# Performance work log

Hardware: AMD Instinct MI355X
Metric: run time of the kernel (lower is better)

## Reference

```python
import jax, jax.numpy as jnp
import numpy as np

B, N, C = 8, 4096, 768
H = 12
D = C // H  # 64


def setup_inputs() -> dict:
    key = jax.random.key(0)
    k1, k2, k3 = jax.random.split(key, 3)
    x = jax.random.normal(k1, (B, N, C), dtype=jnp.float32)
    Wqkv = jax.random.normal(k2, (C, 3 * C), dtype=jnp.float32) * (C ** -0.5)
    Wproj = jax.random.normal(k3, (C, C), dtype=jnp.float32) * (C ** -0.5)
    bproj = jnp.zeros((C,), dtype=jnp.float32)
    return {"x": x, "Wqkv": Wqkv, "Wproj": Wproj, "bproj": bproj}


def reference(x, Wqkv, Wproj, bproj):
    b, n, c = x.shape
    qkv = x @ Wqkv  # [B,N,3C]
    qkv = qkv.reshape(b, n, 3, H, D).transpose(2, 0, 3, 1, 4)  # [3,B,H,N,D]
    q, k, v = qkv[0], qkv[1], qkv[2]
    # softmax over the sequence axis (dim=-2 in torch => N)
    k = jax.nn.softmax(k, axis=-2)
    # context: [B,H,D,D] -- small d x d intermediate
    context = jnp.einsum('bhnd,bhne->bhde', k, v)
    out = jnp.einsum('bhnd,bhde->bhne', q, context)  # [B,H,N,D]
    out = out.transpose(0, 2, 1, 3).reshape(b, n, c)  # b h n d -> b n (h d)
    return out @ Wproj + bproj
```

## Files before the change

kernel.cpp:

```cpp
#include <hip/hip_runtime.h>
#include <cstdint>
#include <cstddef>


typedef __bf16 bf8_t __attribute__((ext_vector_type(8)));
typedef float f4_t __attribute__((ext_vector_type(4)));
typedef float f16_t __attribute__((ext_vector_type(16)));

#define DEV_INLINE __device__ __forceinline__

DEV_INLINE void gload16(const void* g, void* l) {
  __builtin_amdgcn_global_load_lds(
      (const __attribute__((address_space(1))) void*)g,
      (__attribute__((address_space(3))) void*)l, 16, 0, 0);
}

__global__ __launch_bounds__(256) void cast_f32_bf16(const float* __restrict__ in,
                                                     __bf16* __restrict__ out, int n4) {
  int i = blockIdx.x * 256 + threadIdx.x;
  if (i >= n4) return;
  float4 f = ((const float4*)in)[i];
  union { __bf16 h[4]; uint2 u; } o;
  o.h[0] = (__bf16)f.x; o.h[1] = (__bf16)f.y; o.h[2] = (__bf16)f.z; o.h[3] = (__bf16)f.w;
  ((uint2*)out)[i] = o.u;
}

__global__ __launch_bounds__(256) void transpose_cast(const float* __restrict__ in,
                                                      __bf16* __restrict__ out, int R, int C) {
  __shared__ float t[64][65];
  const int tilesR = R >> 6;
  const int tr = blockIdx.x % tilesR, tc = blockIdx.x / tilesR;
  const int tx = threadIdx.x & 63, ty = threadIdx.x >> 6;
  const int r0 = tr * 64, c0 = tc * 64;
#pragma unroll
  for (int p = 0; p < 16; p++) {
    int r = p * 4 + ty;
    t[r][tx] = in[(size_t)(r0 + r) * C + c0 + tx];
  }
  __syncthreads();
#pragma unroll
  for (int p = 0; p < 16; p++) {
    int c = p * 4 + ty;
    out[(size_t)(c0 + c) * R + r0 + tx] = (__bf16)t[tx][c];
  }
}

__global__ __launch_bounds__(256) void wq_cast(const float* __restrict__ in,
                                               __bf16* __restrict__ out) {
  int o = blockIdx.x * 256 + threadIdx.x;
  int r = o / 768, c = o - r * 768;
  out[o] = (__bf16)in[r * 2304 + c];
}

__global__ __launch_bounds__(256) void gemm1_kv(const __bf16* __restrict__ A,
                                                const __bf16* __restrict__ B,
                                                __bf16* __restrict__ KTo,
                                                __bf16* __restrict__ VTo) {
  constexpr int LDA = 768, LDB = 768, KTOT = 768;
  __shared__ __bf16 sA[128 * 32];
  __shared__ __bf16 sB[128 * 32];
  const int tid = threadIdx.x;
  const int xcd = blockIdx.x & 7, g = blockIdx.x >> 3;
  const int mt = xcd * 32 + g / 12, nt = g % 12;
  const int lane = tid & 63, wv = tid >> 6;
  const int wr = (wv >> 1) * 64, wc = (wv & 1) * 64;
  const int l31 = lane & 31, l5 = lane >> 5;

  const int srow = tid >> 2;
  const int sk = ((tid & 3) ^ ((srow >> 1) & 3)) * 8;
  const __bf16* gA = A + (size_t)(mt * 128 + srow) * LDA + sk;
  const __bf16* gB = B + (size_t)(nt * 128 + srow) * LDB + sk;

  const int arow = wr + l31, brow = wc + l31;
  const int asw = (arow >> 1) & 3, bsw = (brow >> 1) & 3;
  const int aoff  = arow * 32 + ((l5 ^ asw) * 8);
  const int aoff2 = arow * 32 + (((2 | l5) ^ asw) * 8);
  const int boff  = brow * 32 + ((l5 ^ bsw) * 8);
  const int boff2 = brow * 32 + (((2 | l5) ^ bsw) * 8);

  f16_t acc[2][2];
#pragma unroll
  for (int i = 0; i < 2; i++)
#pragma unroll
    for (int j = 0; j < 2; j++)
#pragma unroll
      for (int e = 0; e < 16; e++) acc[i][j][e] = 0.f;

  for (int k0 = 0; k0 < KTOT; k0 += 32) {
    gload16(gA, &sA[tid * 8]);
    gload16(gA + 64 * LDA, &sA[tid * 8 + 2048]);
    gload16(gB, &sB[tid * 8]);
    gload16(gB + 64 * LDB, &sB[tid * 8 + 2048]);
    gA += 32; gB += 32;
    __syncthreads();
    bf8_t a0 = *(const bf8_t*)&sA[aoff];
    bf8_t a1 = *(const bf8_t*)&sA[aoff + 1024];
    bf8_t b0 = *(const bf8_t*)&sB[boff];
    bf8_t b1 = *(const bf8_t*)&sB[boff + 1024];
    acc[0][0] = __builtin_amdgcn_mfma_f32_32x32x16_bf16(a0, b0, acc[0][0], 0, 0, 0);
    acc[0][1] = __builtin_amdgcn_mfma_f32_32x32x16_bf16(a0, b1, acc[0][1], 0, 0, 0);
    acc[1][0] = __builtin_amdgcn_mfma_f32_32x32x16_bf16(a1, b0, acc[1][0], 0, 0, 0);
    acc[1][1] = __builtin_amdgcn_mfma_f32_32x32x16_bf16(a1, b1, acc[1][1], 0, 0, 0);
    a0 = *(const bf8_t*)&sA[aoff2];
    a1 = *(const bf8_t*)&sA[aoff2 + 1024];
    b0 = *(const bf8_t*)&sB[boff2];
    b1 = *(const bf8_t*)&sB[boff2 + 1024];
    acc[0][0] = __builtin_amdgcn_mfma_f32_32x32x16_bf16(a0, b0, acc[0][0], 0, 0, 0);
    acc[0][1] = __builtin_amdgcn_mfma_f32_32x32x16_bf16(a0, b1, acc[0][1], 0, 0, 0);
    acc[1][0] = __builtin_amdgcn_mfma_f32_32x32x16_bf16(a1, b0, acc[1][0], 0, 0, 0);
    acc[1][1] = __builtin_amdgcn_mfma_f32_32x32x16_bf16(a1, b1, acc[1][1], 0, 0, 0);
    __syncthreads();
  }

  const int s = nt / 6;
  __bf16* T = (s == 0) ? KTo : VTo;
  const int row0 = mt * 128 + wr;
  const int bidx = row0 >> 12;
  const int n0 = (row0 & 4095) + 4 * l5;
  const int colw0 = (nt % 6) * 128 + wc;
#pragma unroll
  for (int j = 0; j < 2; j++) {
    int cw = colw0 + j * 32 + l31;
    int h = cw >> 6, d = cw & 63;
    __bf16* Tp = &T[((size_t)(bidx * 12 + h) * 64 + d) * 4096];
#pragma unroll
    for (int i = 0; i < 2; i++) {
      int nb = n0 + i * 32;
#pragma unroll
      for (int r2 = 0; r2 < 4; r2++) {
        union { __bf16 h4[4]; uint2 u; } pk;
#pragma unroll
        for (int r = 0; r < 4; r++) pk.h4[r] = (__bf16)acc[i][j][r2 * 4 + r];
        *(uint2*)&Tp[nb + 8 * r2] = pk.u;
      }
    }
  }
}

__global__ __launch_bounds__(256) void stats_rows(const __bf16* __restrict__ KT,
                                                  float2* __restrict__ stats) {
  __shared__ float red[8];
  const __bf16* p = KT + (size_t)blockIdx.x * 4096;
  const int tid = threadIdx.x, lane = tid & 63, wv = tid >> 6;
  bf8_t x0 = *(const bf8_t*)&p[tid * 16];
  bf8_t x1 = *(const bf8_t*)&p[tid * 16 + 8];
  float v[16];
#pragma unroll
  for (int k = 0; k < 8; k++) { v[k] = (float)x0[k]; v[8 + k] = (float)x1[k]; }
  float m = v[0];
#pragma unroll
  for (int k = 1; k < 16; k++) m = fmaxf(m, v[k]);
  for (int o = 32; o; o >>= 1) m = fmaxf(m, __shfl_xor(m, o, 64));
  if (lane == 0) red[wv] = m;
  __syncthreads();
  m = fmaxf(fmaxf(red[0], red[1]), fmaxf(red[2], red[3]));
  float s = 0.f;
#pragma unroll
  for (int k = 0; k < 16; k++) s += __expf(v[k] - m);
  for (int o = 32; o; o >>= 1) s += __shfl_xor(s, o, 64);
  if (lane == 0) red[4 + wv] = s;
  __syncthreads();
  if (tid == 0) {
    float st = red[4] + red[5] + red[6] + red[7];
    stats[blockIdx.x] = make_float2(m, 1.0f / st);
  }
}

__global__ __launch_bounds__(256) void ctx_kernel(const __bf16* __restrict__ KT,
                                                  const __bf16* __restrict__ VT,
                                                  const float2* __restrict__ stats,
                                                  float* __restrict__ part) {
  const int bh = blockIdx.x >> 3, kc = blockIdx.x & 7;
  const int tid = threadIdx.x, lane = tid & 63, wv = tid >> 6;
  const int wr = (wv >> 1) * 32, wc = (wv & 1) * 32;
  const int lr = lane & 15, quad = lane >> 4;
  const __bf16* Ab = KT + (size_t)bh * 64 * 4096;
  const __bf16* Bb = VT + (size_t)bh * 64 * 4096;
  float2 st[2];
  st[0] = stats[bh * 64 + wr + lr];
  st[1] = stats[bh * 64 + wr + 16 + lr];
  const f4_t fz = {0.f, 0.f, 0.f, 0.f};
  f4_t acc[2][2] = {{fz, fz}, {fz, fz}};
  const int kbeg = kc * 512;
  for (int k0 = kbeg; k0 < kbeg + 512; k0 += 32) {
    bf8_t a[2], b[2];
#pragma unroll
    for (int i = 0; i < 2; i++) {
      bf8_t raw = *(const bf8_t*)&Ab[(size_t)(wr + i * 16 + lr) * 4096 + k0 + quad * 8];
#pragma unroll
      for (int e = 0; e < 8; e++)
        a[i][e] = (__bf16)(__expf((float)raw[e] - st[i].x) * st[i].y);
    }
#pragma unroll
    for (int j = 0; j < 2; j++)
      b[j] = *(const bf8_t*)&Bb[(size_t)(wc + j * 16 + lr) * 4096 + k0 + quad * 8];
#pragma unroll
    for (int i = 0; i < 2; i++)
#pragma unroll
      for (int j = 0; j < 2; j++)
        acc[i][j] = __builtin_amdgcn_mfma_f32_16x16x32_bf16(a[i], b[j], acc[i][j], 0, 0, 0);
  }
  float* po = part + (size_t)blockIdx.x * 4096;
#pragma unroll
  for (int i = 0; i < 2; i++)
#pragma unroll
    for (int j = 0; j < 2; j++)
#pragma unroll
      for (int r = 0; r < 4; r++)
        po[(wr + i * 16 + quad * 4 + r) * 64 + wc + j * 16 + lr] = acc[i][j][r];
}

__global__ __launch_bounds__(256) void wfused_kernel(const float* __restrict__ part,
                                                     const __bf16* __restrict__ WpT,
                                                     __bf16* __restrict__ B2T) {
  __shared__ __bf16 sctx[64 * 64];
  const int bh = blockIdx.x, cblk = blockIdx.y;
  const int b = bh / 12, h = bh % 12;
  const int tid = threadIdx.x;
  for (int i = tid; i < 4096; i += 256) {
    float s = 0.f;
#pragma unroll
    for (int kc = 0; kc < 8; kc++) s += part[(size_t)(bh * 8 + kc) * 4096 + i];
    sctx[i] = (__bf16)s;
  }
  __syncthreads();
  const int lane = tid & 63, wv = tid >> 6, lr = lane & 15, quad = lane >> 4;
  const int c0 = cblk * 192 + wv * 48;
  const f4_t fz = {0.f, 0.f, 0.f, 0.f};
  f4_t acc[3][4];
#pragma unroll
  for (int i = 0; i < 3; i++)
#pragma unroll
    for (int j = 0; j < 4; j++) acc[i][j] = fz;
#pragma unroll
  for (int k0 = 0; k0 < 64; k0 += 32) {
    bf8_t a[3], bq[4];
#pragma unroll
    for (int i = 0; i < 3; i++)
      a[i] = *(const bf8_t*)&WpT[(size_t)(c0 + i * 16 + lr) * 768 + h * 64 + k0 + quad * 8];
#pragma unroll
    for (int j = 0; j < 4; j++)
      bq[j] = *(const bf8_t*)&sctx[(j * 16 + lr) * 64 + k0 + quad * 8];
#pragma unroll
    for (int i = 0; i < 3; i++)
#pragma unroll
      for (int j = 0; j < 4; j++)
        acc[i][j] = __builtin_amdgcn_mfma_f32_16x16x32_bf16(a[i], bq[j], acc[i][j], 0, 0, 0);
  }
#pragma unroll
  for (int i = 0; i < 3; i++)
#pragma unroll
    for (int j = 0; j < 4; j++)
#pragma unroll
      for (int r = 0; r < 4; r++) {
        int c = c0 + i * 16 + quad * 4 + r;
        int d = j * 16 + lr;
        B2T[((size_t)b * 768 + c) * 768 + h * 64 + d] = (__bf16)acc[i][j][r];
      }
}

__global__ __launch_bounds__(256) void combine_kernel(const __bf16* __restrict__ B2Tall,
                                                      const __bf16* __restrict__ Wq,
                                                      __bf16* __restrict__ Wcomb) {
  constexpr int LD = 768, BK = 32, KTOT = 768;
  __shared__ __bf16 sA[64 * 32];
  __shared__ __bf16 sB[64 * 32];
  const int b = blockIdx.x / 144, rem = blockIdx.x % 144;
  const int mt = rem / 12, nt = rem % 12;
  const __bf16* A = B2Tall + (size_t)b * 768 * 768;
  const int tid = threadIdx.x, lane = tid & 63, wv = tid >> 6;
  const int wr = (wv >> 1) * 32, wc = (wv & 1) * 32;
  const int lr = lane & 15, quad = lane >> 4;

  const int e0 = tid * 8;
  const int srow = e0 >> 5, skk = e0 & 31;
  const __bf16* gA = A + (size_t)(mt * 64 + srow) * LD + skk;
  const __bf16* gB = Wq + (size_t)(nt * 64 + srow) * LD + skk;

  const f4_t fz = {0.f, 0.f, 0.f, 0.f};
  f4_t acc[2][2] = {{fz, fz}, {fz, fz}};

  for (int k0 = 0; k0 < KTOT; k0 += BK) {
    gload16(gA, &sA[e0]);
    gload16(gB, &sB[e0]);
    gA += BK; gB += BK;
    __syncthreads();
    bf8_t a[2], bq[2];
#pragma unroll
    for (int i = 0; i < 2; i++)
      a[i] = *(const bf8_t*)&sA[(wr + i * 16 + lr) * 32 + quad * 8];
#pragma unroll
    for (int j = 0; j < 2; j++)
      bq[j] = *(const bf8_t*)&sB[(wc + j * 16 + lr) * 32 + quad * 8];
#pragma unroll
    for (int i = 0; i < 2; i++)
#pragma unroll
      for (int j = 0; j < 2; j++)
        acc[i][j] = __builtin_amdgcn_mfma_f32_16x16x32_bf16(a[i], bq[j], acc[i][j], 0, 0, 0);
    __syncthreads();
  }
  __bf16* C = Wcomb + (size_t)b * 768 * 768;
  const int row0 = mt * 64 + wr, col0 = nt * 64 + wc;
#pragma unroll
  for (int i = 0; i < 2; i++)
#pragma unroll
    for (int j = 0; j < 2; j++)
#pragma unroll
      for (int r = 0; r < 4; r++)
        C[(size_t)(row0 + i * 16 + quad * 4 + r) * 768 + col0 + j * 16 + lr] =
            (__bf16)acc[i][j][r];
}

__global__ __launch_bounds__(256) void gemm2_out(const __bf16* __restrict__ A,
                                                 const __bf16* __restrict__ Ball,
                                                 float* __restrict__ C,
                                                 const float* __restrict__ bias) {
  constexpr int LDA = 768, LDB = 768, KTOT = 768;
  __shared__ __bf16 sA[128 * 32];
  __shared__ __bf16 sB[128 * 32];
  const int tid = threadIdx.x;
  const int xcd = blockIdx.x & 7, g = blockIdx.x >> 3;
  const int mt = xcd * 32 + g / 6, nt = g % 6;
  const __bf16* B = Ball + (size_t)(mt >> 5) * 768 * 768;
  const int lane = tid & 63, wv = tid >> 6;
  const int wr = (wv >> 1) * 64, wc = (wv & 1) * 64;
  const int l31 = lane & 31, l5 = lane >> 5;

  const int srow = tid >> 2;
  const int sk = ((tid & 3) ^ ((srow >> 1) & 3)) * 8;
  const __bf16* gA = A + (size_t)(mt * 128 + srow) * LDA + sk;
  const __bf16* gB = B + (size_t)(nt * 128 + srow) * LDB + sk;

  const int arow = wr + l31, brow = wc + l31;
  const int asw = (arow >> 1) & 3, bsw = (brow >> 1) & 3;
  const int aoff  = arow * 32 + ((l5 ^ asw) * 8);
  const int aoff2 = arow * 32 + (((2 | l5) ^ asw) * 8);
  const int boff  = brow * 32 + ((l5 ^ bsw) * 8);
  const int boff2 = brow * 32 + (((2 | l5) ^ bsw) * 8);

  f16_t acc[2][2];
#pragma unroll
  for (int i = 0; i < 2; i++)
#pragma unroll
    for (int j = 0; j < 2; j++)
#pragma unroll
      for (int e = 0; e < 16; e++) acc[i][j][e] = 0.f;

  for (int k0 = 0; k0 < KTOT; k0 += 32) {
    gload16(gA, &sA[tid * 8]);
    gload16(gA + 64 * LDA, &sA[tid * 8 + 2048]);
    gload16(gB, &sB[tid * 8]);
    gload16(gB + 64 * LDB, &sB[tid * 8 + 2048]);
    gA += 32; gB += 32;
    __syncthreads();
    bf8_t a0 = *(const bf8_t*)&sA[aoff];
    bf8_t a1 = *(const bf8_t*)&sA[aoff + 1024];
    bf8_t b0 = *(const bf8_t*)&sB[boff];
    bf8_t b1 = *(const bf8_t*)&sB[boff + 1024];
    acc[0][0] = __builtin_amdgcn_mfma_f32_32x32x16_bf16(a0, b0, acc[0][0], 0, 0, 0);
    acc[0][1] = __builtin_amdgcn_mfma_f32_32x32x16_bf16(a0, b1, acc[0][1], 0, 0, 0);
    acc[1][0] = __builtin_amdgcn_mfma_f32_32x32x16_bf16(a1, b0, acc[1][0], 0, 0, 0);
    acc[1][1] = __builtin_amdgcn_mfma_f32_32x32x16_bf16(a1, b1, acc[1][1], 0, 0, 0);
    a0 = *(const bf8_t*)&sA[aoff2];
    a1 = *(const bf8_t*)&sA[aoff2 + 1024];
    b0 = *(const bf8_t*)&sB[boff2];
    b1 = *(const bf8_t*)&sB[boff2 + 1024];
    acc[0][0] = __builtin_amdgcn_mfma_f32_32x32x16_bf16(a0, b0, acc[0][0], 0, 0, 0);
    acc[0][1] = __builtin_amdgcn_mfma_f32_32x32x16_bf16(a0, b1, acc[0][1], 0, 0, 0);
    acc[1][0] = __builtin_amdgcn_mfma_f32_32x32x16_bf16(a1, b0, acc[1][0], 0, 0, 0);
    acc[1][1] = __builtin_amdgcn_mfma_f32_32x32x16_bf16(a1, b1, acc[1][1], 0, 0, 0);
    __syncthreads();
  }

  const int row0 = mt * 128 + wr + 4 * l5;
  const int col0 = nt * 128 + wc;
#pragma unroll
  for (int j = 0; j < 2; j++) {
    int col = col0 + j * 32 + l31;
    float bv = bias[col];
#pragma unroll
    for (int i = 0; i < 2; i++)
#pragma unroll
      for (int r2 = 0; r2 < 4; r2++) {
        int rbase = row0 + i * 32 + 8 * r2;
#pragma unroll
        for (int r = 0; r < 4; r++)
          C[(size_t)(rbase + r) * 768 + col] = acc[i][j][r2 * 4 + r] + bv;
      }
  }
}

extern "C" void kernel_launch(void* const* d_in, const int* in_sizes, int n_in,
                              void* d_out, int out_size, void* d_ws, size_t ws_size,
                              hipStream_t stream) {
  const float* x = (const float*)d_in[0];
  const float* Wqkv = (const float*)d_in[1];
  const float* Wproj = (const float*)d_in[2];
  const float* bproj = (const float*)d_in[3];
  float* out = (float*)d_out;

  char* ws = (char*)d_ws;
  __bf16* Xb    = (__bf16*)(ws + 0);
  __bf16* KT    = (__bf16*)(ws + 50331648);
  __bf16* VT    = (__bf16*)(ws + 100663296);
  __bf16* WqkvT = (__bf16*)(ws + 150994944);
  float2* stats = (float2*)(ws + 150994944);
  __bf16* Wqc   = (__bf16*)(ws + 154533888);
  __bf16* WpT   = (__bf16*)(ws + 155713536);
  float*  part  = (float*)(ws + 156893184);
  __bf16* B2T   = (__bf16*)(ws + 169476096);
  __bf16* Wcomb = (__bf16*)(ws + 178913280);

  cast_f32_bf16<<<24576, 256, 0, stream>>>(x, Xb, 25165824 / 4);
  transpose_cast<<<12 * 36, 256, 0, stream>>>(Wqkv, WqkvT, 768, 2304);
  wq_cast<<<(768 * 768) / 256, 256, 0, stream>>>(Wqkv, Wqc);
  transpose_cast<<<12 * 12, 256, 0, stream>>>(Wproj, WpT, 768, 768);
  gemm1_kv<<<3072, 256, 0, stream>>>(Xb, WqkvT + 768 * 768, KT, VT);
  stats_rows<<<6144, 256, 0, stream>>>(KT, stats);
  ctx_kernel<<<96 * 8, 256, 0, stream>>>(KT, VT, stats, part);
  wfused_kernel<<<dim3(96, 4), 256, 0, stream>>>(part, WpT, B2T);
  combine_kernel<<<1152, 256, 0, stream>>>(B2T, Wqc, Wcomb);
  gemm2_out<<<1536, 256, 0, stream>>>(Xb, Wcomb, out, bproj);
}
```

Before: 411.8 us.

## Rewrite both large GEMMs with 256x128 tiles and triple-buffered async LDS pipeline

Replaces the single-buffered 128x128 GEMM loop in gemm1_kv and gemm2_out with a shared 512-thread, 256x128-tile main loop. It uses BK=64, a three-stage LDS ring filled by direct global-to-LDS loads, XOR-swizzled layout, and 16x16x32 MFMAs split into four phases with barriers, setprio and vmcnt waits. The aim is to hide global load latency behind MFMA work and raise data reuse per tile. In exchange it uses much more LDS (144KB per block) and more registers, and depends on hand-written waitcnt and barrier choreography.

```diff
diff --git a/kernel.cpp b/kernel.cpp
--- a/kernel.cpp
+++ b/kernel.cpp
@@ -5,7 +5,6 @@
 
 typedef __bf16 bf8_t __attribute__((ext_vector_type(8)));
 typedef float f4_t __attribute__((ext_vector_type(4)));
-typedef float f16_t __attribute__((ext_vector_type(16)));
 
 #define DEV_INLINE __device__ __forceinline__
 
@@ -52,87 +51,111 @@
   out[o] = (__bf16)in[r * 2304 + c];
 }
 
-__global__ __launch_bounds__(256) void gemm1_kv(const __bf16* __restrict__ A,
-                                                const __bf16* __restrict__ B,
-                                                __bf16* __restrict__ KTo,
-                                                __bf16* __restrict__ VTo) {
-  constexpr int LDA = 768, LDB = 768, KTOT = 768;
-  __shared__ __bf16 sA[128 * 32];
-  __shared__ __bf16 sB[128 * 32];
-  const int tid = threadIdx.x;
+
+#define SA_(buf, u, kc) gload16(gA + (size_t)((u) * 64) * 768 + (kc), dAl + (buf) * 16384 + (u) * 4096)
+#define SB_(buf, u, kc) gload16(gB + (size_t)((u) * 64) * 768 + (kc), dBl + (buf) * 8192 + (u) * 4096)
+
+#define PH_(q, STAGE, TAIL) do {                                              \
+    bf8_t af[2][2], bfr[2][2];                                                \
+    _Pragma("unroll") for (int i_ = 0; i_ < 2; i_++)                          \
+      _Pragma("unroll") for (int ks_ = 0; ks_ < 2; ks_++) {                   \
+        af[i_][ks_]  = *(const bf8_t*)(aB + offA[2 * ((q) >> 1) + i_][ks_]);  \
+        bfr[i_][ks_] = *(const bf8_t*)(bB + offB[2 * ((q) & 1) + i_][ks_]);   \
+      }                                                                       \
+    STAGE;                                                                    \
+    __builtin_amdgcn_s_barrier();                                             \
+    __builtin_amdgcn_s_setprio(1);                                            \
+    _Pragma("unroll") for (int ks_ = 0; ks_ < 2; ks_++)                       \
+      _Pragma("unroll") for (int i_ = 0; i_ < 2; i_++)                        \
+        _Pragma("unroll") for (int j_ = 0; j_ < 2; j_++)                      \
+          acc[2 * ((q) >> 1) + i_][2 * ((q) & 1) + j_] =                      \
+            __builtin_amdgcn_mfma_f32_16x16x32_bf16(af[i_][ks_], bfr[j_][ks_],\
+              acc[2 * ((q) >> 1) + i_][2 * ((q) & 1) + j_], 0, 0, 0);         \
+    __builtin_amdgcn_s_setprio(0);                                            \
+    TAIL;                                                                     \
+    __builtin_amdgcn_s_barrier();                                             \
+  } while (0)
+
+#define MAIN_LOOP() do {                                                      \
+    SA_(0, 0, 0); SA_(0, 1, 0); SA_(0, 2, 0); SA_(0, 3, 0);                   \
+    SB_(0, 0, 0); SB_(0, 1, 0);                                               \
+    SA_(1, 0, 64); SA_(1, 1, 64); SA_(1, 2, 64); SA_(1, 3, 64);               \
+    SB_(1, 0, 64); SB_(1, 1, 64);                                             \
+    asm volatile("s_waitcnt vmcnt(6)" ::: "memory");                          \
+    __builtin_amdgcn_s_barrier();                                             \
+    int cur = 0;                                                              \
+    for (int t = 0; t < 10; t++) {                                            \
+      const __bf16* aB = sA + cur * 16384;                                    \
+      const __bf16* bB = sB + cur * 8192;                                     \
+      int nx = cur + 2; if (nx > 2) nx -= 3;                                  \
+      const int kc = (t + 2) * 64;                                            \
+      PH_(0, { SA_(nx, 0, kc); SA_(nx, 1, kc); }, {});                        \
+      PH_(1, { SA_(nx, 2, kc); SA_(nx, 3, kc); }, {});                        \
+      PH_(2, { SB_(nx, 0, kc); }, {});                                        \
+      PH_(3, { SB_(nx, 1, kc); },                                             \
+          { asm volatile("s_waitcnt vmcnt(6)" ::: "memory"); });              \
+      cur++; if (cur > 2) cur = 0;                                            \
+    }                                                                         \
+    { const __bf16* aB = sA + cur * 16384;                                    \
+      const __bf16* bB = sB + cur * 8192;                                     \
+      PH_(0, {}, {}); PH_(1, {}, {}); PH_(2, {}, {});                         \
+      PH_(3, {}, { asm volatile("s_waitcnt vmcnt(0)" ::: "memory"); });       \
+      cur++; if (cur > 2) cur = 0; }                                          \
+    { const __bf16* aB = sA + cur * 16384;                                    \
+      const __bf16* bB = sB + cur * 8192;                                     \
+      PH_(0, {}, {}); PH_(1, {}, {}); PH_(2, {}, {}); PH_(3, {}, {}); }       \
+  } while (0)
+
+#define GEMM_SETUP()                                                          \
+  const int tid = threadIdx.x;                                                \
+  const int trow = tid >> 3;                                                  \
+  const int gcol = ((tid & 7) ^ (trow & 7)) * 8;                              \
+  __bf16* dAl = sA + tid * 8;                                                 \
+  __bf16* dBl = sB + tid * 8;                                                 \
+  const int lane = tid & 63, wv = tid >> 6;                                   \
+  const int wm = wv >> 1, wn = wv & 1;                                        \
+  const int lr = lane & 15, quad = lane >> 4, rsw = lr & 7;                   \
+  int offA[4][2], offB[4][2];                                                 \
+  _Pragma("unroll") for (int f_ = 0; f_ < 4; f_++)                            \
+    _Pragma("unroll") for (int ks_ = 0; ks_ < 2; ks_++) {                     \
+      offA[f_][ks_] = (wm * 64 + f_ * 16 + lr) * 64 + (((ks_ * 4 + quad) ^ rsw) * 8); \
+      offB[f_][ks_] = (wn * 64 + f_ * 16 + lr) * 64 + (((ks_ * 4 + quad) ^ rsw) * 8); \
+    }                                                                         \
+  f4_t acc[4][4];                                                             \
+  _Pragma("unroll") for (int i_ = 0; i_ < 4; i_++)                            \
+    _Pragma("unroll") for (int j_ = 0; j_ < 4; j_++)                          \
+      acc[i_][j_] = (f4_t){0.f, 0.f, 0.f, 0.f};
+
+__global__ __launch_bounds__(512, 2) void gemm1_kv(const __bf16* __restrict__ A,
+                                                   const __bf16* __restrict__ B,
+                                                   __bf16* __restrict__ KTo,
+                                                   __bf16* __restrict__ VTo) {
+  __shared__ __bf16 sA[3 * 16384];
+  __shared__ __bf16 sB[3 * 8192];
   const int xcd = blockIdx.x & 7, g = blockIdx.x >> 3;
-  const int mt = xcd * 32 + g / 12, nt = g % 12;
-  const int lane = tid & 63, wv = tid >> 6;
-  const int wr = (wv >> 1) * 64, wc = (wv & 1) * 64;
-  const int l31 = lane & 31, l5 = lane >> 5;
-
-  const int srow = tid >> 2;
-  const int sk = ((tid & 3) ^ ((srow >> 1) & 3)) * 8;
-  const __bf16* gA = A + (size_t)(mt * 128 + srow) * LDA + sk;
-  const __bf16* gB = B + (size_t)(nt * 128 + srow) * LDB + sk;
-
-  const int arow = wr + l31, brow = wc + l31;
-  const int asw = (arow >> 1) & 3, bsw = (brow >> 1) & 3;
-  const int aoff  = arow * 32 + ((l5 ^ asw) * 8);
-  const int aoff2 = arow * 32 + (((2 | l5) ^ asw) * 8);
-  const int boff  = brow * 32 + ((l5 ^ bsw) * 8);
-  const int boff2 = brow * 32 + (((2 | l5) ^ bsw) * 8);
-
-  f16_t acc[2][2];
-#pragma unroll
-  for (int i = 0; i < 2; i++)
-#pragma unroll
-    for (int j = 0; j < 2; j++)
-#pragma unroll
-      for (int e = 0; e < 16; e++) acc[i][j][e] = 0.f;
-
-  for (int k0 = 0; k0 < KTOT; k0 += 32) {
-    gload16(gA, &sA[tid * 8]);
-    gload16(gA + 64 * LDA, &sA[tid * 8 + 2048]);
-    gload16(gB, &sB[tid * 8]);
-    gload16(gB + 64 * LDB, &sB[tid * 8 + 2048]);
-    gA += 32; gB += 32;
-    __syncthreads();
-    bf8_t a0 = *(const bf8_t*)&sA[aoff];
-    bf8_t a1 = *(const bf8_t*)&sA[aoff + 1024];
-    bf8_t b0 = *(const bf8_t*)&sB[boff];
-    bf8_t b1 = *(const bf8_t*)&sB[boff + 1024];
-    acc[0][0] = __builtin_amdgcn_mfma_f32_32x32x16_bf16(a0, b0, acc[0][0], 0, 0, 0);
-    acc[0][1] = __builtin_amdgcn_mfma_f32_32x32x16_bf16(a0, b1, acc[0][1], 0, 0, 0);
-    acc[1][0] = __builtin_amdgcn_mfma_f32_32x32x16_bf16(a1, b0, acc[1][0], 0, 0, 0);
-    acc[1][1] = __builtin_amdgcn_mfma_f32_32x32x16_bf16(a1, b1, acc[1][1], 0, 0, 0);
-    a0 = *(const bf8_t*)&sA[aoff2];
-    a1 = *(const bf8_t*)&sA[aoff2 + 1024];
-    b0 = *(const bf8_t*)&sB[boff2];
-    b1 = *(const bf8_t*)&sB[boff2 + 1024];
-    acc[0][0] = __builtin_amdgcn_mfma_f32_32x32x16_bf16(a0, b0, acc[0][0], 0, 0, 0);
-    acc[0][1] = __builtin_amdgcn_mfma_f32_32x32x16_bf16(a0, b1, acc[0][1], 0, 0, 0);
-    acc[1][0] = __builtin_amdgcn_mfma_f32_32x32x16_bf16(a1, b0, acc[1][0], 0, 0, 0);
-    acc[1][1] = __builtin_amdgcn_mfma_f32_32x32x16_bf16(a1, b1, acc[1][1], 0, 0, 0);
-    __syncthreads();
-  }
+  const int mt = xcd * 16 + g / 12, nt = g % 12;
+  GEMM_SETUP();
+  const __bf16* gA = A + (size_t)(mt * 256 + trow) * 768 + gcol;
+  const __bf16* gB = B + (size_t)(nt * 128 + trow) * 768 + gcol;
+
+  MAIN_LOOP();
 
   const int s = nt / 6;
-  __bf16* T = (s == 0) ? KTo : VTo;
-  const int row0 = mt * 128 + wr;
-  const int bidx = row0 >> 12;
-  const int n0 = (row0 & 4095) + 4 * l5;
-  const int colw0 = (nt % 6) * 128 + wc;
-#pragma unroll
-  for (int j = 0; j < 2; j++) {
-    int cw = colw0 + j * 32 + l31;
-    int h = cw >> 6, d = cw & 63;
-    __bf16* Tp = &T[((size_t)(bidx * 12 + h) * 64 + d) * 4096];
-#pragma unroll
-    for (int i = 0; i < 2; i++) {
-      int nb = n0 + i * 32;
-#pragma unroll
-      for (int r2 = 0; r2 < 4; r2++) {
-        union { __bf16 h4[4]; uint2 u; } pk;
-#pragma unroll
-        for (int r = 0; r < 4; r++) pk.h4[r] = (__bf16)acc[i][j][r2 * 4 + r];
-        *(uint2*)&Tp[nb + 8 * r2] = pk.u;
-      }
+  __bf16* T = s ? VTo : KTo;
+  const int colbase = (nt % 6) * 128 + wn * 64;
+  const int bidx = mt >> 4;
+  const int nbase = (mt & 15) * 256 + wm * 64 + quad * 4;
+#pragma unroll
+  for (int ci = 0; ci < 4; ci++) {
+    int col = colbase + ci * 16 + lr;
+    int h = col >> 6, d = col & 63;
+    __bf16* Tp = T + ((size_t)(bidx * 12 + h) * 64 + d) * 4096;
+#pragma unroll
+    for (int ri = 0; ri < 4; ri++) {
+      union { __bf16 h4[4]; uint2 u2; } pk;
+#pragma unroll
+      for (int r = 0; r < 4; r++) pk.h4[r] = (__bf16)acc[ri][ci][r];
+      *(uint2*)&Tp[nbase + ri * 16] = pk.u2;
     }
   }
 }
@@ -263,8 +286,8 @@
                                                       const __bf16* __restrict__ Wq,
                                                       __bf16* __restrict__ Wcomb) {
   constexpr int LD = 768, BK = 32, KTOT = 768;
-  __shared__ __bf16 sA[64 * 32];
-  __shared__ __bf16 sB[64 * 32];
+  __shared__ __bf16 sAc[64 * 32];
+  __shared__ __bf16 sBc[64 * 32];
   const int b = blockIdx.x / 144, rem = blockIdx.x % 144;
   const int mt = rem / 12, nt = rem % 12;
   const __bf16* A = B2Tall + (size_t)b * 768 * 768;
@@ -281,17 +304,17 @@
   f4_t acc[2][2] = {{fz, fz}, {fz, fz}};
 
   for (int k0 = 0; k0 < KTOT; k0 += BK) {
-    gload16(gA, &sA[e0]);
-    gload16(gB, &sB[e0]);
+    gload16(gA, &sAc[e0]);
+    gload16(gB, &sBc[e0]);
     gA += BK; gB += BK;
     __syncthreads();
     bf8_t a[2], bq[2];
 #pragma unroll
     for (int i = 0; i < 2; i++)
-      a[i] = *(const bf8_t*)&sA[(wr + i * 16 + lr) * 32 + quad * 8];
+      a[i] = *(const bf8_t*)&sAc[(wr + i * 16 + lr) * 32 + quad * 8];
 #pragma unroll
     for (int j = 0; j < 2; j++)
-      bq[j] = *(const bf8_t*)&sB[(wc + j * 16 + lr) * 32 + quad * 8];
+      bq[j] = *(const bf8_t*)&sBc[(wc + j * 16 + lr) * 32 + quad * 8];
 #pragma unroll
     for (int i = 0; i < 2; i++)
 #pragma unroll
@@ -311,82 +334,33 @@
             (__bf16)acc[i][j][r];
 }
 
-__global__ __launch_bounds__(256) void gemm2_out(const __bf16* __restrict__ A,
-                                                 const __bf16* __restrict__ Ball,
-                                                 float* __restrict__ C,
-                                                 const float* __restrict__ bias) {
-  constexpr int LDA = 768, LDB = 768, KTOT = 768;
-  __shared__ __bf16 sA[128 * 32];
-  __shared__ __bf16 sB[128 * 32];
-  const int tid = threadIdx.x;
+__global__ __launch_bounds__(512, 2) void gemm2_out(const __bf16* __restrict__ A,
+                                                    const __bf16* __restrict__ Ball,
+                                                    float* __restrict__ C,
+                                                    const float* __restrict__ bias) {
+  __shared__ __bf16 sA[3 * 16384];
+  __shared__ __bf16 sB[3 * 8192];
   const int xcd = blockIdx.x & 7, g = blockIdx.x >> 3;
-  const int mt = xcd * 32 + g / 6, nt = g % 6;
-  const __bf16* B = Ball + (size_t)(mt >> 5) * 768 * 768;
-  const int lane = tid & 63, wv = tid >> 6;
-  const int wr = (wv >> 1) * 64, wc = (wv & 1) * 64;
-  const int l31 = lane & 31, l5 = lane >> 5;
-
-  const int srow = tid >> 2;
-  const int sk = ((tid & 3) ^ ((srow >> 1) & 3)) * 8;
-  const __bf16* gA = A + (size_t)(mt * 128 + srow) * LDA + sk;
-  const __bf16* gB = B + (size_t)(nt * 128 + srow) * LDB + sk;
-
-  const int arow = wr + l31, brow = wc + l31;
-  const int asw = (arow >> 1) & 3, bsw = (brow >> 1) & 3;
-  const int aoff  = arow * 32 + ((l5 ^ asw) * 8);
-  const int aoff2 = arow * 32 + (((2 | l5) ^ asw) * 8);
-  const int boff  = brow * 32 + ((l5 ^ bsw) * 8);
-  const int boff2 = brow * 32 + (((2 | l5) ^ bsw) * 8);
-
-  f16_t acc[2][2];
-#pragma unroll
-  for (int i = 0; i < 2; i++)
-#pragma unroll
-    for (int j = 0; j < 2; j++)
-#pragma unroll
-      for (int e = 0; e < 16; e++) acc[i][j][e] = 0.f;
-
-  for (int k0 = 0; k0 < KTOT; k0 += 32) {
-    gload16(gA, &sA[tid * 8]);
-    gload16(gA + 64 * LDA, &sA[tid * 8 + 2048]);
-    gload16(gB, &sB[tid * 8]);
-    gload16(gB + 64 * LDB, &sB[tid * 8 + 2048]);
-    gA += 32; gB += 32;
-    __syncthreads();
-    bf8_t a0 = *(const bf8_t*)&sA[aoff];
-    bf8_t a1 = *(const bf8_t*)&sA[aoff + 1024];
-    bf8_t b0 = *(const bf8_t*)&sB[boff];
-    bf8_t b1 = *(const bf8_t*)&sB[boff + 1024];
-    acc[0][0] = __builtin_amdgcn_mfma_f32_32x32x16_bf16(a0, b0, acc[0][0], 0, 0, 0);
-    acc[0][1] = __builtin_amdgcn_mfma_f32_32x32x16_bf16(a0, b1, acc[0][1], 0, 0, 0);
-    acc[1][0] = __builtin_amdgcn_mfma_f32_32x32x16_bf16(a1, b0, acc[1][0], 0, 0, 0);
-    acc[1][1] = __builtin_amdgcn_mfma_f32_32x32x16_bf16(a1, b1, acc[1][1], 0, 0, 0);
-    a0 = *(const bf8_t*)&sA[aoff2];
-    a1 = *(const bf8_t*)&sA[aoff2 + 1024];
-    b0 = *(const bf8_t*)&sB[boff2];
-    b1 = *(const bf8_t*)&sB[boff2 + 1024];
-    acc[0][0] = __builtin_amdgcn_mfma_f32_32x32x16_bf16(a0, b0, acc[0][0], 0, 0, 0);
-    acc[0][1] = __builtin_amdgcn_mfma_f32_32x32x16_bf16(a0, b1, acc[0][1], 0, 0, 0);
-    acc[1][0] = __builtin_amdgcn_mfma_f32_32x32x16_bf16(a1, b0, acc[1][0], 0, 0, 0);
-    acc[1][1] = __builtin_amdgcn_mfma_f32_32x32x16_bf16(a1, b1, acc[1][1], 0, 0, 0);
-    __syncthreads();
-  }
-
-  const int row0 = mt * 128 + wr + 4 * l5;
-  const int col0 = nt * 128 + wc;
-#pragma unroll
-  for (int j = 0; j < 2; j++) {
-    int col = col0 + j * 32 + l31;
+  const int mt = xcd * 16 + g / 6, nt = g % 6;
+  const __bf16* B = Ball + (size_t)(mt >> 4) * 768 * 768;
+  GEMM_SETUP();
+  const __bf16* gA = A + (size_t)(mt * 256 + trow) * 768 + gcol;
+  const __bf16* gB = B + (size_t)(nt * 128 + trow) * 768 + gcol;
+
+  MAIN_LOOP();
+
+  const int row0 = mt * 256 + wm * 64 + quad * 4;
+  const int col0 = nt * 128 + wn * 64;
+#pragma unroll
+  for (int ci = 0; ci < 4; ci++) {
+    int col = col0 + ci * 16 + lr;
     float bv = bias[col];
 #pragma unroll
-    for (int i = 0; i < 2; i++)
-#pragma unroll
-      for (int r2 = 0; r2 < 4; r2++) {
-        int rbase = row0 + i * 32 + 8 * r2;
-#pragma unroll
-        for (int r = 0; r < 4; r++)
-          C[(size_t)(rbase + r) * 768 + col] = acc[i][j][r2 * 4 + r] + bv;
-      }
+    for (int ri = 0; ri < 4; ri++) {
+#pragma unroll
+      for (int r = 0; r < 4; r++)
+        C[(size_t)(row0 + ri * 16 + r) * 768 + col] = acc[ri][ci][r] + bv;
+    }
   }
 }
 
@@ -415,10 +389,10 @@
   transpose_cast<<<12 * 36, 256, 0, stream>>>(Wqkv, WqkvT, 768, 2304);
   wq_cast<<<(768 * 768) / 256, 256, 0, stream>>>(Wqkv, Wqc);
   transpose_cast<<<12 * 12, 256, 0, stream>>>(Wproj, WpT, 768, 768);
-  gemm1_kv<<<3072, 256, 0, stream>>>(Xb, WqkvT + 768 * 768, KT, VT);
+  gemm1_kv<<<1536, 512, 0, stream>>>(Xb, WqkvT + 768 * 768, KT, VT);
   stats_rows<<<6144, 256, 0, stream>>>(KT, stats);
   ctx_kernel<<<96 * 8, 256, 0, stream>>>(KT, VT, stats, part);
   wfused_kernel<<<dim3(96, 4), 256, 0, stream>>>(part, WpT, B2T);
   combine_kernel<<<1152, 256, 0, stream>>>(B2T, Wqc, Wcomb);
-  gemm2_out<<<1536, 256, 0, stream>>>(Xb, Wcomb, out, bproj);
-}
+  gemm2_out<<<768, 512, 0, stream>>>(Xb, Wcomb, out, bproj);
+}
```

New measurement: 438.6 us. +6.5%, slower.
